# Kernel optimization log

Measured on AMD Instinct MI355X. Metric: run time of the kernel, lower is better.

Reference implementation:

```python
import jax, jax.numpy as jnp
import numpy as np

B, T, V, D, H, DK = 64, 384, 12, 256, 4, 64

def _ln(x, g, b):
    m = jnp.mean(x, -1, keepdims=True)
    v = jnp.var(x, -1, keepdims=True)
    return (x - m) * jax.lax.rsqrt(v + 1e-5) * g + b

def _grn(x, W1, b1, W2, b2, Wg, bg, lng, lnb, ctx=None, Wc=None, Ws=None, bs=None):
    # eta2 = ELU(fc1(x) + ctx_proj(ctx)); eta1 = fc2(eta2); GLU; residual; LN
    h = x @ W1 + b1
    if ctx is not None:
        h = h + ctx @ Wc
    h = jax.nn.elu(h)
    h = h @ W2 + b2
    g = h @ Wg + bg
    a, gate = jnp.split(g, 2, axis=-1)
    gated = a * jax.nn.sigmoid(gate)
    skip = x if Ws is None else x @ Ws + bs
    return _ln(skip + gated, lng, lnb)

def setup_inputs() -> dict:
    key = jax.random.key(0)
    ks = iter(jax.random.split(key, 48))
    def rn(shape, s=0.02):
        return jax.random.normal(next(ks), shape, jnp.float32) * s
    return {
        'x': jax.random.normal(next(ks), (B, T, V, D), jnp.float32),
        'context': jax.random.normal(next(ks), (B, D), jnp.float32),
        # flattened GRN of VSN: in=V*D, hidden=D, out=V, context=D, skip needed
        'fg_W1': rn((V * D, D)), 'fg_b1': jnp.zeros((D,), jnp.float32),
        'fg_Wc': rn((D, D)),
        'fg_W2': rn((D, D)), 'fg_b2': jnp.zeros((D,), jnp.float32),
        'fg_Wg': rn((D, 2 * V)), 'fg_bg': jnp.zeros((2 * V,), jnp.float32),
        'fg_Ws': rn((V * D, V)), 'fg_bs': jnp.zeros((V,), jnp.float32),
        'fg_lng': jnp.ones((V,), jnp.float32), 'fg_lnb': jnp.zeros((V,), jnp.float32),
        # per-variable GRNs (V of them, in=out=hidden=D, no skip/ctx), stacked
        'sv_W1': rn((V, D, D)), 'sv_b1': jnp.zeros((V, D), jnp.float32),
        'sv_W2': rn((V, D, D)), 'sv_b2': jnp.zeros((V, D), jnp.float32),
        'sv_Wg': rn((V, D, 2 * D)), 'sv_bg': jnp.zeros((V, 2 * D), jnp.float32),
        'sv_lng': jnp.ones((V, D), jnp.float32), 'sv_lnb': jnp.zeros((V, D), jnp.float32),
        # static enrichment GRN: in=out=hidden=D with context
        'en_W1': rn((D, D)), 'en_b1': jnp.zeros((D,), jnp.float32),
        'en_Wc': rn((D, D)),
        'en_W2': rn((D, D)), 'en_b2': jnp.zeros((D,), jnp.float32),
        'en_Wg': rn((D, 2 * D)), 'en_bg': jnp.zeros((2 * D,), jnp.float32),
        'en_lng': jnp.ones((D,), jnp.float32), 'en_lnb': jnp.zeros((D,), jnp.float32),
        # interpretable MHA: per-head Q/K, shared V, output proj
        'Wq': rn((H, D, DK)), 'Wk': rn((H, D, DK)),
        'Wv': rn((D, DK)), 'Wo': rn((DK, D)),
    }

def reference(x, context, fg_W1, fg_b1, fg_Wc, fg_W2, fg_b2, fg_Wg, fg_bg, fg_Ws, fg_bs,
              fg_lng, fg_lnb, sv_W1, sv_b1, sv_W2, sv_b2, sv_Wg, sv_bg, sv_lng, sv_lnb,
              en_W1, en_b1, en_Wc, en_W2, en_b2, en_Wg, en_bg, en_lng, en_lnb,
              Wq, Wk, Wv, Wo):
    b, t, v, d = x.shape
    ctx3 = context[:, None, :]  # broadcast static context over time
    # ---- Variable Selection Network ----
    xf = x.reshape(b, t, v * d)
    w = _grn(xf, fg_W1, fg_b1, fg_W2, fg_b2, fg_Wg, fg_bg, fg_lng, fg_lnb,
             ctx=ctx3, Wc=fg_Wc, Ws=fg_Ws, bs=fg_bs)
    w = jax.nn.softmax(w, axis=-1)  # (b,t,v)
    per_var = jax.vmap(_grn, in_axes=(2, 0, 0, 0, 0, 0, 0, 0, 0), out_axes=2)(
        x, sv_W1, sv_b1, sv_W2, sv_b2, sv_Wg, sv_bg, sv_lng, sv_lnb)  # (b,t,v,d)
    sel = jnp.sum(per_var * w[..., None], axis=2)  # (b,t,d)
    # ---- static enrichment GRN ----
    enr = _grn(sel, en_W1, en_b1, en_W2, en_b2, en_Wg, en_bg, en_lng, en_lnb,
               ctx=ctx3, Wc=en_Wc)
    # ---- interpretable multi-head attention (causal), per-head Q/K, shared V ----
    q = jnp.einsum('btd,hdk->hbtk', enr, Wq)
    k = jnp.einsum('btd,hdk->hbtk', enr, Wk)
    vp = enr @ Wv  # (b,t,dk), shared across heads
    scale = jax.lax.rsqrt(jnp.asarray(DK, jnp.float32))
    scores = jnp.einsum('hbqd,hbkd->hbqk', q, k) * scale
    mask = jnp.triu(jnp.ones((t, t), bool), 1)  # True = masked (future)
    scores = jnp.where(mask, jnp.asarray(-1e9, scores.dtype), scores)
    attn = jax.nn.softmax(scores, axis=-1)
    heads = jnp.einsum('hbqk,bkd->hbqd', attn, vp)
    out = jnp.mean(heads, axis=0) @ Wo  # mean over heads then shared output proj
    return out
```

## Files before the change

kernel.cpp:

```cpp
#include <hip/hip_runtime.h>
#include <hip/hip_bf16.h>
#include <stdint.h>
#include <stddef.h>

typedef __bf16 bf16;
typedef __bf16 bf16x8 __attribute__((ext_vector_type(8)));
typedef float  f32x4  __attribute__((ext_vector_type(4)));

#define BTR 24576
#define EPI_BIAS  1
#define EPI_CVEC  2
#define EPI_ELU   4
#define EPI_ATTN  8
#define EPI_GATE  32
#define EPI_PERM  64

__device__ __forceinline__ int perm512(int n) {
  return (n < 256) ? (((n >> 4) << 5) + (n & 15))
                   : ((((n - 256) >> 4) << 5) + ((n - 256) & 15) + 16);
}

template<int EPI, bool AF32, bool CF32>
__global__ __launch_bounds__(256, 2)
void gemm_kernel(const void* __restrict__ Av, int lda, long sAh, long sAb,
                 const bf16* __restrict__ Bt, int ldb, long sBh, long sBb,
                 void* __restrict__ Cv, int ldc, long sC,
                 int K, int zdiv,
                 const float* __restrict__ bias, const float* __restrict__ cvec,
                 long sBias)
{
  __shared__ __align__(16) bf16 As[128 * 32];
  __shared__ __align__(16) bf16 Bs[128 * 32];

  const int tid  = threadIdx.x;
  const int wave = tid >> 6, lane = tid & 63;
  const int wr = wave >> 1, wc = wave & 1;
  const int quad = lane >> 4, l16 = lane & 15;

  const int z  = blockIdx.z;
  const int hh = z / zdiv, bb = z % zdiv;
  const float* AbF = nullptr; const bf16* AbH = nullptr;
  if constexpr (AF32) AbF = (const float*)Av + (long)hh * sAh + (long)bb * sAb;
  else                AbH = (const bf16*)Av  + (long)hh * sAh + (long)bb * sAb;
  const bf16* Bb = Bt + (long)hh * sBh + (long)bb * sBb;
  float* CbF = nullptr; bf16* CbH = nullptr;
  if constexpr (CF32) CbF = (float*)Cv + (long)z * sC;
  else                CbH = (bf16*)Cv  + (long)z * sC;

  const int rowBase = blockIdx.y * 128;
  const int colBase = blockIdx.x * 128;

  f32x4 acc[4][4];
#pragma unroll
  for (int i = 0; i < 4; ++i)
#pragma unroll
    for (int j = 0; j < 4; ++j) { acc[i][j][0]=0.f; acc[i][j][1]=0.f; acc[i][j][2]=0.f; acc[i][j][3]=0.f; }

  const int r0 = tid >> 2, kc = tid & 3;
  const int r1 = tid >> 1, kh = (tid & 1) * 16;
  const int arow = (wr * 64 + l16) * 32 + quad * 8;
  const int brow = (wc * 64 + l16) * 32 + quad * 8;

  for (int k0 = 0; k0 < K; k0 += 32) {
    bf16x8 a0, a1;
    if constexpr (AF32) {
      const float* p = AbF + (size_t)(rowBase + r1) * lda + k0 + kh;
      f32x4 f0 = *(const f32x4*)(p);
      f32x4 f1 = *(const f32x4*)(p + 4);
      f32x4 f2 = *(const f32x4*)(p + 8);
      f32x4 f3 = *(const f32x4*)(p + 12);
#pragma unroll
      for (int e = 0; e < 4; ++e) {
        a0[e] = (bf16)f0[e]; a0[4 + e] = (bf16)f1[e];
        a1[e] = (bf16)f2[e]; a1[4 + e] = (bf16)f3[e];
      }
    } else {
      a0 = *(const bf16x8*)(AbH + (size_t)(rowBase + r0)      * lda + k0 + kc * 8);
      a1 = *(const bf16x8*)(AbH + (size_t)(rowBase + 64 + r0) * lda + k0 + kc * 8);
    }
    bf16x8 b0 = *(const bf16x8*)(Bb + (size_t)(colBase + r0)      * ldb + k0 + kc * 8);
    bf16x8 b1 = *(const bf16x8*)(Bb + (size_t)(colBase + 64 + r0) * ldb + k0 + kc * 8);
    __syncthreads();
    if constexpr (AF32) {
      *(bf16x8*)(As + r1 * 32 + kh)     = a0;
      *(bf16x8*)(As + r1 * 32 + kh + 8) = a1;
    } else {
      *(bf16x8*)(As +        r0 * 32 + kc * 8) = a0;
      *(bf16x8*)(As + 2048 + r0 * 32 + kc * 8) = a1;
    }
    *(bf16x8*)(Bs +        r0 * 32 + kc * 8) = b0;
    *(bf16x8*)(Bs + 2048 + r0 * 32 + kc * 8) = b1;
    __syncthreads();

    bf16x8 af[4], bfv[4];
#pragma unroll
    for (int mi = 0; mi < 4; ++mi) af[mi]  = *(const bf16x8*)(As + arow + mi * 512);
#pragma unroll
    for (int ni = 0; ni < 4; ++ni) bfv[ni] = *(const bf16x8*)(Bs + brow + ni * 512);
#pragma unroll
    for (int mi = 0; mi < 4; ++mi)
#pragma unroll
      for (int ni = 0; ni < 4; ++ni)
        acc[mi][ni] = __builtin_amdgcn_mfma_f32_16x16x32_bf16(af[mi], bfv[ni], acc[mi][ni], 0, 0, 0);
  }

  if constexpr (EPI & EPI_GATE) {
    const float* bp = bias + (size_t)z * sBias;
#pragma unroll
    for (int mi = 0; mi < 4; ++mi) {
#pragma unroll
      for (int nj = 0; nj < 2; ++nj) {
        const int ni = nj * 2;
        const int pa = colBase + wc * 64 + ni * 16 + l16;
        const int j  = (colBase >> 1) + wc * 32 + nj * 16 + l16;
        const float ba = bp[pa], bg = bp[pa + 16];
        const int row0 = rowBase + wr * 64 + mi * 16 + quad * 4;
#pragma unroll
        for (int r = 0; r < 4; ++r) {
          float a = acc[mi][ni][r]     + ba;
          float g = acc[mi][ni + 1][r] + bg;
          CbH[(size_t)(row0 + r) * ldc + j] = (bf16)(a / (1.f + __expf(-g)));
        }
      }
    }
    return;
  }
  const int bctx = (EPI & EPI_CVEC) ? (rowBase / 384) : 0;
  const float* bp = (EPI & EPI_BIAS) ? bias + (size_t)z * sBias : nullptr;
#pragma unroll
  for (int mi = 0; mi < 4; ++mi) {
#pragma unroll
    for (int ni = 0; ni < 4; ++ni) {
      const int row0 = rowBase + wr * 64 + mi * 16 + quad * 4;
      const int col  = colBase + wc * 64 + ni * 16 + l16;
      float bv = (EPI & EPI_BIAS) ? bp[col] : 0.f;
      float cv = (EPI & EPI_CVEC) ? cvec[bctx * 256 + col] : 0.f;
#pragma unroll
      for (int r = 0; r < 4; ++r) {
        float v = acc[mi][ni][r] + bv + cv;
        if (EPI & EPI_ELU)  v = v > 0.f ? v : __expf(v) - 1.f;
        if (EPI & EPI_ATTN) { v *= 0.125f; if (col > row0 + r) v = -1e9f; }
        int srow = row0 + r;
        if constexpr (EPI & EPI_PERM) srow = perm512(srow);
        if constexpr (CF32) CbF[(size_t)srow * ldc + col] = v;
        else                CbH[(size_t)srow * ldc + col] = (bf16)v;
      }
    }
  }
}

__global__ __launch_bounds__(512, 2)
void fgwide_kernel(const float* __restrict__ A, const bf16* __restrict__ Bt,
                   bf16* __restrict__ C, const float* __restrict__ bias,
                   const float* __restrict__ cvec)
{
  __shared__ __align__(16) bf16 As[128 * 32];
  __shared__ __align__(16) bf16 Bs[384 * 32];
  const int tid = threadIdx.x;
  const int wave = tid >> 6, lane = tid & 63;
  const int wr = wave >> 2, wc4 = wave & 3;
  const int quad = lane >> 4, l16 = lane & 15;
  const int rowBase = blockIdx.x * 128;

  f32x4 acc[4][6];
#pragma unroll
  for (int i = 0; i < 4; ++i)
#pragma unroll
    for (int j = 0; j < 6; ++j) { acc[i][j][0]=0.f; acc[i][j][1]=0.f; acc[i][j][2]=0.f; acc[i][j][3]=0.f; }

  const int r1 = tid >> 2, kh = (tid & 3) * 8;
  const int arow = (wr * 64 + l16) * 32 + quad * 8;
  const int brow = (wc4 * 96 + l16) * 32 + quad * 8;

  for (int k0 = 0; k0 < 3072; k0 += 32) {
    const float* p = A + (size_t)(rowBase + r1) * 3072 + k0 + kh;
    f32x4 f0 = *(const f32x4*)(p);
    f32x4 f1 = *(const f32x4*)(p + 4);
    bf16x8 av;
#pragma unroll
    for (int e = 0; e < 4; ++e) { av[e] = (bf16)f0[e]; av[4 + e] = (bf16)f1[e]; }
    bf16x8 bv[3];
#pragma unroll
    for (int c = 0; c < 3; ++c) {
      int idx = c * 512 + tid;
      int rb = idx >> 2, kc = idx & 3;
      bv[c] = *(const bf16x8*)(Bt + (size_t)rb * 3072 + k0 + kc * 8);
    }
    __syncthreads();
    *(bf16x8*)(As + r1 * 32 + kh) = av;
#pragma unroll
    for (int c = 0; c < 3; ++c) {
      int idx = c * 512 + tid;
      int rb = idx >> 2, kc = idx & 3;
      *(bf16x8*)(Bs + rb * 32 + kc * 8) = bv[c];
    }
    __syncthreads();

    bf16x8 af[4], bfv[6];
#pragma unroll
    for (int mi = 0; mi < 4; ++mi) af[mi]  = *(const bf16x8*)(As + arow + mi * 512);
#pragma unroll
    for (int ni = 0; ni < 6; ++ni) bfv[ni] = *(const bf16x8*)(Bs + brow + ni * 512);
#pragma unroll
    for (int mi = 0; mi < 4; ++mi)
#pragma unroll
      for (int ni = 0; ni < 6; ++ni)
        acc[mi][ni] = __builtin_amdgcn_mfma_f32_16x16x32_bf16(af[mi], bfv[ni], acc[mi][ni], 0, 0, 0);
  }

  const int bctx = rowBase / 384;
#pragma unroll
  for (int mi = 0; mi < 4; ++mi) {
#pragma unroll
    for (int ni = 0; ni < 6; ++ni) {
      const int col = wc4 * 96 + ni * 16 + l16;
      const bool act = (wc4 * 96 + ni * 16) < 256;
      const float bv = bias[col];
      const float cv = act ? cvec[bctx * 256 + col] : 0.f;
      const int row0 = rowBase + wr * 64 + mi * 16 + quad * 4;
#pragma unroll
      for (int r = 0; r < 4; ++r) {
        float v = acc[mi][ni][r] + bv + cv;
        if (act) v = v > 0.f ? v : __expf(v) - 1.f;
        C[(size_t)(row0 + r) * 384 + col] = (bf16)v;
      }
    }
  }
}

__global__ void prep_kernel(
    const float* fgW1, const float* fgWs, const float* fgW2, const float* fgWg,
    const float* fgb1, const float* fgbs,
    const float* svW1, const float* svWg, const float* svW2,
    const float* enW1, const float* enWg, const float* enW2,
    const float* Wq, const float* Wk, const float* Wv, const float* Wo,
    bf16* fgW1WsT, bf16* fgWgPT, bf16* fgW2C, float* bias384,
    bf16* svW1T, bf16* svWgT, bf16* svW2C,
    bf16* enW1T, bf16* enWgT, bf16* enW2C,
    bf16* WqkvT, bf16* WoT)
{
  long i = (long)blockIdx.x * 256 + threadIdx.x;
  if (i < 1179648) {
    int n = i / 3072, k = i % 3072; float v;
    if (n < 256) v = fgW1[(size_t)k * 256 + n];
    else { int nn = n - 256; v = (nn < 12) ? fgWs[(size_t)k * 12 + nn] : 0.f; }
    fgW1WsT[i] = (bf16)v; return; } i -= 1179648;
  if (i < 32768)  { int n = i >> 8, k = i & 255; fgWgPT[i] = (n < 24) ? (bf16)fgWg[k * 24 + n] : (bf16)0.f; return; } i -= 32768;
  if (i < 65536)  { fgW2C[i] = (bf16)fgW2[i]; return; } i -= 65536;
  if (i < 384)    { bias384[i] = (i < 256) ? fgb1[i] : ((i < 268) ? fgbs[i - 256] : 0.f); return; } i -= 384;
  if (i < 786432) { long v = i >> 16, r = i & 65535; int n = r >> 8, k = r & 255; svW1T[i] = (bf16)svW1[(v << 16) + k * 256 + n]; return; } i -= 786432;
  if (i < 1572864){ long v = i >> 17, r = i & 131071; int n = r >> 8, k = r & 255; svWgT[i] = (bf16)svWg[(v << 17) + k * 512 + n]; return; } i -= 1572864;
  if (i < 786432) { svW2C[i] = (bf16)svW2[i]; return; } i -= 786432;
  if (i < 65536)  { int n = i >> 8, k = i & 255; enW1T[i] = (bf16)enW1[k * 256 + n]; return; } i -= 65536;
  if (i < 131072) { int n = i >> 8, k = i & 255; enWgT[i] = (bf16)enWg[k * 512 + n]; return; } i -= 131072;
  if (i < 65536)  { enW2C[i] = (bf16)enW2[i]; return; } i -= 65536;
  if (i < 163840) { int n = i >> 8, k = i & 255; float val;
                    if (n < 256)      val = Wq[(n >> 6) * 16384 + k * 64 + (n & 63)];
                    else if (n < 512) { int nn = n - 256; val = Wk[(nn >> 6) * 16384 + k * 64 + (nn & 63)]; }
                    else if (n < 576) val = Wv[k * 64 + (n - 512)];
                    else              val = 0.f;
                    WqkvT[i] = (bf16)val; return; } i -= 163840;
  if (i < 16384)  { int n = i >> 6, k = i & 63; WoT[i] = (bf16)Wo[k * 256 + n]; }
}

__global__ void biasfuse_kernel(const float* fgb2, const float* fgWg, const float* fgbg,
                                const float* svb2, const float* svWg, const float* svbg,
                                const float* enb2, const float* enWg, const float* enbg,
                                float* fgBF, float* svBFP, float* enBFP)
{
  int i = blockIdx.x * 256 + threadIdx.x;
  if (i < 128) {
    float s = 0.f;
    if (i < 24) { s = fgbg[i]; for (int k = 0; k < 256; ++k) s += fgb2[k] * fgWg[k * 24 + i]; }
    fgBF[i] = s; return; } i -= 128;
  if (i < 6144) {
    int v = i >> 9, n = i & 511;
    float s = svbg[v * 512 + n];
    const float* W = svWg + (size_t)v * 131072;
    const float* b2 = svb2 + v * 256;
    for (int k = 0; k < 256; ++k) s += b2[k] * W[k * 512 + n];
    svBFP[v * 512 + perm512(n)] = s; return; } i -= 6144;
  if (i < 512) {
    float s = enbg[i];
    for (int k = 0; k < 256; ++k) s += enb2[k] * enWg[k * 512 + i];
    enBFP[perm512(i)] = s; }
}

__global__ void cvec_kernel(const float* __restrict__ ctx, const float* __restrict__ WcFg,
                            const float* __restrict__ WcEn, float* __restrict__ outFg,
                            float* __restrict__ outEn) {
  int b = blockIdx.x, n = threadIdx.x;
  const float* Wc = blockIdx.y ? WcEn : WcFg;
  float* o = blockIdx.y ? outEn : outFg;
  float acc = 0.f;
  for (int d = 0; d < 256; ++d) acc += ctx[b * 256 + d] * Wc[d * 256 + n];
  o[b * 256 + n] = acc;
}

__global__ void lnsm12_kernel(const bf16* __restrict__ B384, const bf16* __restrict__ GP,
                              const float* __restrict__ lng, const float* __restrict__ lnb,
                              float* __restrict__ w) {
  int r = blockIdx.x * 256 + threadIdx.x;
  if (r >= BTR) return;
  float y[12]; float m = 0.f;
#pragma unroll
  for (int j = 0; j < 12; ++j) {
    float a = (float)GP[(size_t)r * 128 + j];
    float g = (float)GP[(size_t)r * 128 + 12 + j];
    float gated = a / (1.f + __expf(-g));
    y[j] = (float)B384[(size_t)r * 384 + 256 + j] + gated; m += y[j];
  }
  m *= (1.f / 12.f);
  float var = 0.f;
#pragma unroll
  for (int j = 0; j < 12; ++j) { float d = y[j] - m; var += d * d; }
  var *= (1.f / 12.f);
  float rstd = rsqrtf(var + 1e-5f);
  float mx = -1e30f;
#pragma unroll
  for (int j = 0; j < 12; ++j) { y[j] = (y[j] - m) * rstd * lng[j] + lnb[j]; mx = fmaxf(mx, y[j]); }
  float s = 0.f;
#pragma unroll
  for (int j = 0; j < 12; ++j) { y[j] = __expf(y[j] - mx); s += y[j]; }
  float inv = 1.f / s;
#pragma unroll
  for (int j = 0; j < 12; ++j) w[r * 12 + j] = y[j] * inv;
}

__device__ __forceinline__ void block_sum2(float a, float b, float& oa, float& ob) {
#pragma unroll
  for (int o = 32; o; o >>= 1) { a += __shfl_xor(a, o); b += __shfl_xor(b, o); }
  __shared__ float ra[4], rb[4];
  int w = threadIdx.x >> 6;
  if ((threadIdx.x & 63) == 0) { ra[w] = a; rb[w] = b; }
  __syncthreads();
  oa = ra[0] + ra[1] + ra[2] + ra[3];
  ob = rb[0] + rb[1] + rb[2] + rb[3];
  __syncthreads();
}

__global__ __launch_bounds__(256)
void selacc4_kernel(const bf16* __restrict__ GATED, const float* __restrict__ x,
                    const float* __restrict__ w, const float* __restrict__ lng,
                    const float* __restrict__ lnb, float* __restrict__ sel,
                    bf16* __restrict__ selb, int v0, int isFirst, int isLast) {
  int r = blockIdx.x, d = threadIdx.x;
  float acc = isFirst ? 0.f : sel[(size_t)r * 256 + d];
#pragma unroll
  for (int vv = 0; vv < 4; ++vv) {
    int v = v0 + vv;
    float gated = (float)GATED[(size_t)vv * ((size_t)BTR * 256) + (size_t)r * 256 + d];
    float y = x[(size_t)r * 3072 + v * 256 + d] + gated;
    float s1, s2;
    block_sum2(y, y * y, s1, s2);
    float mean = s1 * (1.f / 256.f);
    float var  = s2 * (1.f / 256.f) - mean * mean;
    float val  = (y - mean) * rsqrtf(var + 1e-5f) * lng[v * 256 + d] + lnb[v * 256 + d];
    acc += w[r * 12 + v] * val;
  }
  if (isLast) selb[(size_t)r * 256 + d] = (bf16)acc;
  else        sel[(size_t)r * 256 + d] = acc;
}

__global__ __launch_bounds__(256)
void enrln_kernel(const bf16* __restrict__ GATED, const bf16* __restrict__ skip,
                  const float* __restrict__ lng, const float* __restrict__ lnb,
                  bf16* __restrict__ out) {
  int r = blockIdx.x, d = threadIdx.x;
  float gated = (float)GATED[(size_t)r * 256 + d];
  float y = (float)skip[(size_t)r * 256 + d] + gated;
  float s1, s2;
  block_sum2(y, y * y, s1, s2);
  float mean = s1 * (1.f / 256.f);
  float var = s2 * (1.f / 256.f) - mean * mean;
  float norm = (y - mean) * rsqrtf(var + 1e-5f);
  out[(size_t)r * 256 + d] = (bf16)(norm * lng[d] + lnb[d]);
}

__global__ __launch_bounds__(384)
void softmax_avg_kernel(const bf16* __restrict__ S, bf16* __restrict__ P) {
  const int bq = blockIdx.x;
  const int b = bq / 384, q = bq % 384;
  const int j = threadIdx.x;
  const int w = j >> 6;
  __shared__ float red[6];
  float pb = 0.f;
  for (int h = 0; h < 4; ++h) {
    float s = (float)S[((size_t)((h * 64 + b) * 384 + q)) * 384 + j];
    float m = s;
#pragma unroll
    for (int o = 32; o; o >>= 1) m = fmaxf(m, __shfl_xor(m, o));
    if ((j & 63) == 0) red[w] = m;
    __syncthreads();
    m = fmaxf(fmaxf(fmaxf(red[0], red[1]), fmaxf(red[2], red[3])), fmaxf(red[4], red[5]));
    __syncthreads();
    float e = __expf(s - m);
    float l = e;
#pragma unroll
    for (int o = 32; o; o >>= 1) l += __shfl_xor(l, o);
    if ((j & 63) == 0) red[w] = l;
    __syncthreads();
    l = red[0] + red[1] + red[2] + red[3] + red[4] + red[5];
    __syncthreads();
    pb += e / l;
  }
  P[(size_t)bq * 384 + j] = (bf16)(0.25f * pb);
}

__global__ void transpose_u_kernel(const bf16* __restrict__ U, bf16* __restrict__ UT) {
  int t = blockIdx.x, b = blockIdx.y, d = threadIdx.x;
  UT[((size_t)b * 256 + d) * 384 + t] = U[((size_t)b * 384 + t) * 256 + d];
}

template<int EPI, bool AF32, bool CF32>
static inline void rungemm(hipStream_t s,
    const void* A, int lda, const bf16* Bt, int ldb, void* C, int ldc,
    int M, int N, int K,
    const float* bias = nullptr, const float* cvec = nullptr,
    int Z = 1, int zdiv = 1,
    long sAh = 0, long sAb = 0, long sBh = 0, long sBb = 0, long sC = 0, long sBias = 0)
{
  dim3 grid(N / 128, M / 128, Z);
  gemm_kernel<EPI, AF32, CF32><<<grid, 256, 0, s>>>(A, lda, sAh, sAb, Bt, ldb, sBh, sBb, C, ldc, sC, K, zdiv, bias, cvec, sBias);
}

extern "C" void kernel_launch(void* const* d_in, const int* in_sizes, int n_in,
                              void* d_out, int out_size, void* d_ws, size_t ws_size,
                              hipStream_t stream)
{
  (void)in_sizes; (void)n_in; (void)out_size;
  const float* x      = (const float*)d_in[0];
  const float* ctx    = (const float*)d_in[1];
  const float* fg_W1  = (const float*)d_in[2];
  const float* fg_b1  = (const float*)d_in[3];
  const float* fg_Wc  = (const float*)d_in[4];
  const float* fg_W2  = (const float*)d_in[5];
  const float* fg_b2  = (const float*)d_in[6];
  const float* fg_Wg  = (const float*)d_in[7];
  const float* fg_bg  = (const float*)d_in[8];
  const float* fg_Ws  = (const float*)d_in[9];
  const float* fg_bs  = (const float*)d_in[10];
  const float* fg_lng = (const float*)d_in[11];
  const float* fg_lnb = (const float*)d_in[12];
  const float* sv_W1  = (const float*)d_in[13];
  const float* sv_b1  = (const float*)d_in[14];
  const float* sv_W2  = (const float*)d_in[15];
  const float* sv_b2  = (const float*)d_in[16];
  const float* sv_Wg  = (const float*)d_in[17];
  const float* sv_bg  = (const float*)d_in[18];
  const float* sv_lng = (const float*)d_in[19];
  const float* sv_lnb = (const float*)d_in[20];
  const float* en_W1  = (const float*)d_in[21];
  const float* en_b1  = (const float*)d_in[22];
  const float* en_Wc  = (const float*)d_in[23];
  const float* en_W2  = (const float*)d_in[24];
  const float* en_b2  = (const float*)d_in[25];
  const float* en_Wg  = (const float*)d_in[26];
  const float* en_bg  = (const float*)d_in[27];
  const float* en_lng = (const float*)d_in[28];
  const float* en_lnb = (const float*)d_in[29];
  const float* Wq     = (const float*)d_in[30];
  const float* Wk     = (const float*)d_in[31];
  const float* Wv     = (const float*)d_in[32];
  const float* Wo     = (const float*)d_in[33];

  static constexpr size_t OFF_FGW1WST = 0;
  static constexpr size_t OFF_FGWGPT  = OFF_FGW1WST + 2359296;
  static constexpr size_t OFF_FGW2C   = OFF_FGWGPT  + 65536;
  static constexpr size_t OFF_FGW2GT  = OFF_FGW2C   + 131072;
  static constexpr size_t OFF_BIAS384 = OFF_FGW2GT  + 65536;
  static constexpr size_t OFF_FGBF    = OFF_BIAS384 + 1536;
  static constexpr size_t OFF_SVW1T   = OFF_FGBF    + 512;
  static constexpr size_t OFF_SVWGT   = OFF_SVW1T   + 1572864;
  static constexpr size_t OFF_SVW2C   = OFF_SVWGT   + 3145728;
  static constexpr size_t OFF_SVW2GPT = OFF_SVW2C   + 1572864;
  static constexpr size_t OFF_SVBFP   = OFF_SVW2GPT + 3145728;
  static constexpr size_t OFF_ENW1T   = OFF_SVBFP   + 24576;
  static constexpr size_t OFF_ENWGT   = OFF_ENW1T   + 131072;
  static constexpr size_t OFF_ENW2C   = OFF_ENWGT   + 262144;
  static constexpr size_t OFF_ENW2GPT = OFF_ENW2C   + 131072;
  static constexpr size_t OFF_ENBFP   = OFF_ENW2GPT + 262144;
  static constexpr size_t OFF_WQKVT   = OFF_ENBFP   + 2048;
  static constexpr size_t OFF_WOT     = OFF_WQKVT   + 327680;
  static constexpr size_t OFF_CVECFG  = OFF_WOT     + 32768;
  static constexpr size_t OFF_CVECEN  = OFF_CVECFG  + 65536;
  static constexpr size_t ARENA       = OFF_CVECEN  + 65536;
  static constexpr size_t WS_NEEDED = ARENA + 152174592;

  if (ws_size < WS_NEEDED) return;

  char* ws = (char*)d_ws;
  bf16*  fgW1WsT = (bf16*)(ws + OFF_FGW1WST);
  bf16*  fgWgPT  = (bf16*)(ws + OFF_FGWGPT);
  bf16*  fgW2C   = (bf16*)(ws + OFF_FGW2C);
  bf16*  fgW2gT  = (bf16*)(ws + OFF_FGW2GT);
  float* bias384 = (float*)(ws + OFF_BIAS384);
  float* fgBF    = (float*)(ws + OFF_FGBF);
  bf16*  svW1T   = (bf16*)(ws + OFF_SVW1T);
  bf16*  svWgT   = (bf16*)(ws + OFF_SVWGT);
  bf16*  svW2C   = (bf16*)(ws + OFF_SVW2C);
  bf16*  svW2gPT = (bf16*)(ws + OFF_SVW2GPT);
  float* svBFP   = (float*)(ws + OFF_SVBFP);
  bf16*  enW1T   = (bf16*)(ws + OFF_ENW1T);
  bf16*  enWgT   = (bf16*)(ws + OFF_ENWGT);
  bf16*  enW2C   = (bf16*)(ws + OFF_ENW2C);
  bf16*  enW2gPT = (bf16*)(ws + OFF_ENW2GPT);
  float* enBFP   = (float*)(ws + OFF_ENBFP);
  bf16*  WqkvT   = (bf16*)(ws + OFF_WQKVT);
  bf16*  WoT     = (bf16*)(ws + OFF_WOT);
  float* cvecFg  = (float*)(ws + OFF_CVECFG);
  float* cvecEn  = (float*)(ws + OFF_CVECEN);
  char*  ar      = ws + ARENA;
  float* sel     = (float*)(ar + 0);
  bf16*  selb    = (bf16*)(ar + 25165824);
  float* wbuf    = (float*)(ar + 37748736);
  bf16*  H1G     = (bf16*)(ar + 38928384);
  bf16*  BUF384  = (bf16*)(ar + 38928384);
  bf16*  GPAD    = (bf16*)(ar + 57802752);
  bf16*  H1EN    = (bf16*)(ar + 38928384);
  bf16*  GATED   = (bf16*)(ar + 89260032);
  bf16*  GATEDEN = (bf16*)(ar + 89260032);
  bf16*  enr     = (bf16*)(ar + 139591680);
  bf16*  QKV     = (bf16*)(ar + 0);
  bf16*  Pbar    = (bf16*)(ar + 38928384);
  bf16*  Sbuf    = (bf16*)(ar + 64094208);
  bf16*  U       = (bf16*)(ar + 139591680);
  bf16*  UT      = (bf16*)(ar + 64094208);
  float* out     = (float*)d_out;

  prep_kernel<<<19010, 256, 0, stream>>>(fg_W1, fg_Ws, fg_W2, fg_Wg, fg_b1, fg_bs,
                                         sv_W1, sv_Wg, sv_W2, en_W1, en_Wg, en_W2,
                                         Wq, Wk, Wv, Wo,
                                         fgW1WsT, fgWgPT, fgW2C, bias384,
                                         svW1T, svWgT, svW2C, enW1T, enWgT, enW2C,
                                         WqkvT, WoT);
  biasfuse_kernel<<<27, 256, 0, stream>>>(fg_b2, fg_Wg, fg_bg, sv_b2, sv_Wg, sv_bg,
                                          en_b2, en_Wg, en_bg, fgBF, svBFP, enBFP);
  cvec_kernel<<<dim3(64, 2), 256, 0, stream>>>(ctx, fg_Wc, en_Wc, cvecFg, cvecEn);

  rungemm<0,        false, false>(stream, fgWgPT, 256, fgW2C, 256, fgW2gT, 256, 128, 256, 256);
  rungemm<EPI_PERM, false, false>(stream, svWgT, 256, svW2C, 256, svW2gPT, 256, 512, 256, 256,
                                  nullptr, nullptr, 12, 12, 0, 131072, 0, 65536, 131072);
  rungemm<EPI_PERM, false, false>(stream, enWgT, 256, enW2C, 256, enW2gPT, 256, 512, 256, 256);

  fgwide_kernel<<<192, 512, 0, stream>>>(x, fgW1WsT, BUF384, bias384, cvecFg);
  rungemm<EPI_BIAS, false, false>(stream, BUF384, 384, fgW2gT, 256, GPAD, 128, BTR, 128, 256, fgBF);
  lnsm12_kernel<<<96, 256, 0, stream>>>(BUF384, GPAD, fg_lng, fg_lnb, wbuf);

  for (int g = 0; g < 3; ++g) {
    rungemm<EPI_BIAS|EPI_ELU, true, false>(
        stream, x + g * 4 * 256, 3072, svW1T + (size_t)g * 4 * 65536, 256, H1G, 256, BTR, 256, 256,
        sv_b1 + g * 4 * 256, nullptr, 4, 4, 0, 256, 0, 65536, (long)BTR * 256, 256);
    rungemm<EPI_BIAS|EPI_GATE, false, false>(
        stream, H1G, 256, svW2gPT + (size_t)g * 4 * 131072, 256, GATED, 256, BTR, 512, 256,
        svBFP + g * 4 * 512, nullptr, 4, 4, 0, (long)BTR * 256, 0, 131072, (long)BTR * 256, 512);
    selacc4_kernel<<<BTR, 256, 0, stream>>>(GATED, x, wbuf, sv_lng, sv_lnb, sel, selb,
                                            g * 4, g == 0, g == 2);
  }

  rungemm<EPI_BIAS|EPI_CVEC|EPI_ELU, false, false>(stream, selb, 256, enW1T, 256, H1EN, 256, BTR, 256, 256, en_b1, cvecEn);
  rungemm<EPI_BIAS|EPI_GATE, false, false>(stream, H1EN, 256, enW2gPT, 256, GATEDEN, 256, BTR, 512, 256, enBFP);
  enrln_kernel<<<BTR, 256, 0, stream>>>(GATEDEN, selb, en_lng, en_lnb, enr);

  rungemm<0, false, false>(stream, enr, 256, WqkvT, 256, QKV, 640, BTR, 640, 256);
  rungemm<EPI_ATTN, false, false>(stream, QKV, 640, QKV + 256, 640, Sbuf, 384, 384, 384, 64,
                                  nullptr, nullptr, 256, 64, 64, 245760L, 64, 245760L, 147456L);
  softmax_avg_kernel<<<BTR, 384, 0, stream>>>(Sbuf, Pbar);
  rungemm<0, false, false>(stream, QKV + 512, 640, WoT, 64, U, 256, BTR, 256, 64);
  transpose_u_kernel<<<dim3(384, 64), 256, 0, stream>>>(U, UT);
  rungemm<0, false, true>(stream, Pbar, 384, UT, 384, out, 256, 384, 256, 384,
                          nullptr, nullptr, 64, 1, 147456L, 0, 98304L, 0, 98304L);
}
```

Measured before the change: 1.418 ms.

## Prefetch next K-tile in GEMMs, shrink fgwide tiles, drop U transpose

The generic GEMM and the wide fg GEMM now load the next K-slice into registers while the current slice's MFMAs run, so global latency overlaps compute. The fgwide kernel moves from 128-row, 512-thread blocks to 64-row, 256-thread blocks, doubling the block count for better occupancy. The Wv·Wo projection is now computed directly in transposed layout by swapping GEMM operands, which removes the separate transpose kernel and its intermediate buffer. Prefetching holds more live registers per thread, and the smaller fgwide tile reloads B more often.

```diff
diff --git a/kernel.cpp b/kernel.cpp
--- a/kernel.cpp
+++ b/kernel.cpp
@@ -61,36 +61,51 @@
   const int arow = (wr * 64 + l16) * 32 + quad * 8;
   const int brow = (wc * 64 + l16) * 32 + quad * 8;
 
+  f32x4 pf0, pf1, pf2, pf3;
+  bf16x8 pa0, pa1, pb0, pb1;
+  if constexpr (AF32) {
+    const float* p = AbF + (size_t)(rowBase + r1) * lda + kh;
+    pf0 = *(const f32x4*)(p);     pf1 = *(const f32x4*)(p + 4);
+    pf2 = *(const f32x4*)(p + 8); pf3 = *(const f32x4*)(p + 12);
+  } else {
+    pa0 = *(const bf16x8*)(AbH + (size_t)(rowBase + r0)      * lda + kc * 8);
+    pa1 = *(const bf16x8*)(AbH + (size_t)(rowBase + 64 + r0) * lda + kc * 8);
+  }
+  pb0 = *(const bf16x8*)(Bb + (size_t)(colBase + r0)      * ldb + kc * 8);
+  pb1 = *(const bf16x8*)(Bb + (size_t)(colBase + 64 + r0) * ldb + kc * 8);
+
   for (int k0 = 0; k0 < K; k0 += 32) {
-    bf16x8 a0, a1;
+    __syncthreads();
     if constexpr (AF32) {
-      const float* p = AbF + (size_t)(rowBase + r1) * lda + k0 + kh;
-      f32x4 f0 = *(const f32x4*)(p);
-      f32x4 f1 = *(const f32x4*)(p + 4);
-      f32x4 f2 = *(const f32x4*)(p + 8);
-      f32x4 f3 = *(const f32x4*)(p + 12);
+      bf16x8 a0, a1;
 #pragma unroll
       for (int e = 0; e < 4; ++e) {
-        a0[e] = (bf16)f0[e]; a0[4 + e] = (bf16)f1[e];
-        a1[e] = (bf16)f2[e]; a1[4 + e] = (bf16)f3[e];
+        a0[e] = (bf16)pf0[e]; a0[4 + e] = (bf16)pf1[e];
+        a1[e] = (bf16)pf2[e]; a1[4 + e] = (bf16)pf3[e];
       }
-    } else {
-      a0 = *(const bf16x8*)(AbH + (size_t)(rowBase + r0)      * lda + k0 + kc * 8);
-      a1 = *(const bf16x8*)(AbH + (size_t)(rowBase + 64 + r0) * lda + k0 + kc * 8);
-    }
-    bf16x8 b0 = *(const bf16x8*)(Bb + (size_t)(colBase + r0)      * ldb + k0 + kc * 8);
-    bf16x8 b1 = *(const bf16x8*)(Bb + (size_t)(colBase + 64 + r0) * ldb + k0 + kc * 8);
-    __syncthreads();
-    if constexpr (AF32) {
       *(bf16x8*)(As + r1 * 32 + kh)     = a0;
       *(bf16x8*)(As + r1 * 32 + kh + 8) = a1;
     } else {
-      *(bf16x8*)(As +        r0 * 32 + kc * 8) = a0;
-      *(bf16x8*)(As + 2048 + r0 * 32 + kc * 8) = a1;
-    }
-    *(bf16x8*)(Bs +        r0 * 32 + kc * 8) = b0;
-    *(bf16x8*)(Bs + 2048 + r0 * 32 + kc * 8) = b1;
-    __syncthreads();
+      *(bf16x8*)(As +        r0 * 32 + kc * 8) = pa0;
+      *(bf16x8*)(As + 2048 + r0 * 32 + kc * 8) = pa1;
+    }
+    *(bf16x8*)(Bs +        r0 * 32 + kc * 8) = pb0;
+    *(bf16x8*)(Bs + 2048 + r0 * 32 + kc * 8) = pb1;
+    __syncthreads();
+
+    const int k1 = k0 + 32;
+    if (k1 < K) {
+      if constexpr (AF32) {
+        const float* p = AbF + (size_t)(rowBase + r1) * lda + k1 + kh;
+        pf0 = *(const f32x4*)(p);     pf1 = *(const f32x4*)(p + 4);
+        pf2 = *(const f32x4*)(p + 8); pf3 = *(const f32x4*)(p + 12);
+      } else {
+        pa0 = *(const bf16x8*)(AbH + (size_t)(rowBase + r0)      * lda + k1 + kc * 8);
+        pa1 = *(const bf16x8*)(AbH + (size_t)(rowBase + 64 + r0) * lda + k1 + kc * 8);
+      }
+      pb0 = *(const bf16x8*)(Bb + (size_t)(colBase + r0)      * ldb + k1 + kc * 8);
+      pb1 = *(const bf16x8*)(Bb + (size_t)(colBase + 64 + r0) * ldb + k1 + kc * 8);
+    }
 
     bf16x8 af[4], bfv[4];
 #pragma unroll
@@ -149,18 +164,17 @@
   }
 }
 
-__global__ __launch_bounds__(512, 2)
+__global__ __launch_bounds__(256, 2)
 void fgwide_kernel(const float* __restrict__ A, const bf16* __restrict__ Bt,
                    bf16* __restrict__ C, const float* __restrict__ bias,
                    const float* __restrict__ cvec)
 {
-  __shared__ __align__(16) bf16 As[128 * 32];
+  __shared__ __align__(16) bf16 As[64 * 32];
   __shared__ __align__(16) bf16 Bs[384 * 32];
   const int tid = threadIdx.x;
   const int wave = tid >> 6, lane = tid & 63;
-  const int wr = wave >> 2, wc4 = wave & 3;
   const int quad = lane >> 4, l16 = lane & 15;
-  const int rowBase = blockIdx.x * 128;
+  const int rowBase = blockIdx.x * 64;
 
   f32x4 acc[4][6];
 #pragma unroll
@@ -169,32 +183,43 @@
     for (int j = 0; j < 6; ++j) { acc[i][j][0]=0.f; acc[i][j][1]=0.f; acc[i][j][2]=0.f; acc[i][j][3]=0.f; }
 
   const int r1 = tid >> 2, kh = (tid & 3) * 8;
-  const int arow = (wr * 64 + l16) * 32 + quad * 8;
-  const int brow = (wc4 * 96 + l16) * 32 + quad * 8;
-
+  const int arow = l16 * 32 + quad * 8;
+  const int brow = (wave * 96 + l16) * 32 + quad * 8;
+
+  f32x4 pf0, pf1;
+  bf16x8 pbv[6];
+  {
+    const float* p = A + (size_t)(rowBase + r1) * 3072 + kh;
+    pf0 = *(const f32x4*)(p); pf1 = *(const f32x4*)(p + 4);
+#pragma unroll
+    for (int c = 0; c < 6; ++c) {
+      const int idx = c * 256 + tid, rb = idx >> 2, kc2 = idx & 3;
+      pbv[c] = *(const bf16x8*)(Bt + (size_t)rb * 3072 + kc2 * 8);
+    }
+  }
   for (int k0 = 0; k0 < 3072; k0 += 32) {
-    const float* p = A + (size_t)(rowBase + r1) * 3072 + k0 + kh;
-    f32x4 f0 = *(const f32x4*)(p);
-    f32x4 f1 = *(const f32x4*)(p + 4);
+    __syncthreads();
     bf16x8 av;
 #pragma unroll
-    for (int e = 0; e < 4; ++e) { av[e] = (bf16)f0[e]; av[4 + e] = (bf16)f1[e]; }
-    bf16x8 bv[3];
-#pragma unroll
-    for (int c = 0; c < 3; ++c) {
-      int idx = c * 512 + tid;
-      int rb = idx >> 2, kc = idx & 3;
-      bv[c] = *(const bf16x8*)(Bt + (size_t)rb * 3072 + k0 + kc * 8);
-    }
-    __syncthreads();
+    for (int e = 0; e < 4; ++e) { av[e] = (bf16)pf0[e]; av[4 + e] = (bf16)pf1[e]; }
     *(bf16x8*)(As + r1 * 32 + kh) = av;
 #pragma unroll
-    for (int c = 0; c < 3; ++c) {
-      int idx = c * 512 + tid;
-      int rb = idx >> 2, kc = idx & 3;
-      *(bf16x8*)(Bs + rb * 32 + kc * 8) = bv[c];
-    }
-    __syncthreads();
+    for (int c = 0; c < 6; ++c) {
+      const int idx = c * 256 + tid, rb = idx >> 2, kc2 = idx & 3;
+      *(bf16x8*)(Bs + rb * 32 + kc2 * 8) = pbv[c];
+    }
+    __syncthreads();
+
+    const int k1 = k0 + 32;
+    if (k1 < 3072) {
+      const float* p = A + (size_t)(rowBase + r1) * 3072 + k1 + kh;
+      pf0 = *(const f32x4*)(p); pf1 = *(const f32x4*)(p + 4);
+#pragma unroll
+      for (int c = 0; c < 6; ++c) {
+        const int idx = c * 256 + tid, rb = idx >> 2, kc2 = idx & 3;
+        pbv[c] = *(const bf16x8*)(Bt + (size_t)rb * 3072 + k1 + kc2 * 8);
+      }
+    }
 
     bf16x8 af[4], bfv[6];
 #pragma unroll
@@ -213,11 +238,11 @@
   for (int mi = 0; mi < 4; ++mi) {
 #pragma unroll
     for (int ni = 0; ni < 6; ++ni) {
-      const int col = wc4 * 96 + ni * 16 + l16;
-      const bool act = (wc4 * 96 + ni * 16) < 256;
+      const int col = wave * 96 + ni * 16 + l16;
+      const bool act = (wave * 96 + ni * 16) < 256;
       const float bv = bias[col];
       const float cv = act ? cvec[bctx * 256 + col] : 0.f;
-      const int row0 = rowBase + wr * 64 + mi * 16 + quad * 4;
+      const int row0 = rowBase + mi * 16 + quad * 4;
 #pragma unroll
       for (int r = 0; r < 4; ++r) {
         float v = acc[mi][ni][r] + bv + cv;
@@ -405,11 +430,6 @@
     pb += e / l;
   }
   P[(size_t)bq * 384 + j] = (bf16)(0.25f * pb);
-}
-
-__global__ void transpose_u_kernel(const bf16* __restrict__ U, bf16* __restrict__ UT) {
-  int t = blockIdx.x, b = blockIdx.y, d = threadIdx.x;
-  UT[((size_t)b * 256 + d) * 384 + t] = U[((size_t)b * 384 + t) * 256 + d];
 }
 
 template<int EPI, bool AF32, bool CF32>
@@ -524,7 +544,6 @@
   bf16*  QKV     = (bf16*)(ar + 0);
   bf16*  Pbar    = (bf16*)(ar + 38928384);
   bf16*  Sbuf    = (bf16*)(ar + 64094208);
-  bf16*  U       = (bf16*)(ar + 139591680);
   bf16*  UT      = (bf16*)(ar + 64094208);
   float* out     = (float*)d_out;
 
@@ -543,7 +562,7 @@
                                   nullptr, nullptr, 12, 12, 0, 131072, 0, 65536, 131072);
   rungemm<EPI_PERM, false, false>(stream, enWgT, 256, enW2C, 256, enW2gPT, 256, 512, 256, 256);
 
-  fgwide_kernel<<<192, 512, 0, stream>>>(x, fgW1WsT, BUF384, bias384, cvecFg);
+  fgwide_kernel<<<384, 256, 0, stream>>>(x, fgW1WsT, BUF384, bias384, cvecFg);
   rungemm<EPI_BIAS, false, false>(stream, BUF384, 384, fgW2gT, 256, GPAD, 128, BTR, 128, 256, fgBF);
   lnsm12_kernel<<<96, 256, 0, stream>>>(BUF384, GPAD, fg_lng, fg_lnb, wbuf);
 
@@ -566,8 +585,8 @@
   rungemm<EPI_ATTN, false, false>(stream, QKV, 640, QKV + 256, 640, Sbuf, 384, 384, 384, 64,
                                   nullptr, nullptr, 256, 64, 64, 245760L, 64, 245760L, 147456L);
   softmax_avg_kernel<<<BTR, 384, 0, stream>>>(Sbuf, Pbar);
-  rungemm<0, false, false>(stream, QKV + 512, 640, WoT, 64, U, 256, BTR, 256, 64);
-  transpose_u_kernel<<<dim3(384, 64), 256, 0, stream>>>(U, UT);
+  rungemm<0, false, false>(stream, WoT, 64, QKV + 512, 640, UT, 384, 256, 384, 64,
+                           nullptr, nullptr, 64, 64, 0, 0, 0, 245760L, 98304L);
   rungemm<0, false, true>(stream, Pbar, 384, UT, 384, out, 256, 384, 256, 384,
                           nullptr, nullptr, 64, 1, 147456L, 0, 98304L, 0, 98304L);
 }
```

Result: faster. 1.357 ms (-4.3%).
